# Optimization experiments

Hardware: AMD Instinct MI355X
Metric: run time of the kernel (lower is better)

The kernel has to match this reference:

```python
import jax, jax.numpy as jnp
import numpy as np

B, T, F, H, P, HEADS = 1024, 128, 9, 256, 2048, 4
DH = H // HEADS

def _lstm_layer(x, Wih, Whh, bih, bhh):
    # x: [B,T,in]; gate order i,f,g,o (torch convention)
    xp = jnp.einsum('bti,gi->btg', x, Wih) + bih + bhh  # [B,T,4H]
    h0 = jnp.zeros((x.shape[0], Whh.shape[1]), x.dtype)
    def step(carry, xt):
        h, c = carry
        g = xt + h @ Whh.T
        i, f, gg, o = jnp.split(g, 4, axis=-1)
        c = jax.nn.sigmoid(f) * c + jax.nn.sigmoid(i) * jnp.tanh(gg)
        h = jax.nn.sigmoid(o) * jnp.tanh(c)
        return (h, c), h
    _, hs = jax.lax.scan(step, (h0, h0), jnp.swapaxes(xp, 0, 1))
    return jnp.swapaxes(hs, 0, 1)  # [B,T,H]

def _layernorm(x, g, b, eps=1e-5):
    mu = x.mean(-1, keepdims=True)
    var = ((x - mu) ** 2).mean(-1, keepdims=True)
    return (x - mu) * jax.lax.rsqrt(var + eps) * g + b

def setup_inputs():
    key = jax.random.key(0)
    ks = jax.random.split(key, 30)
    w = lambda k, s: jax.random.normal(k, s, jnp.float32) * 0.05
    return {
        'x': jax.random.normal(ks[0], (B, T, F), jnp.float32),
        'sku_indices': jnp.arange(B, dtype=jnp.int32),
        'adj': jax.random.uniform(ks[1], (P, P), jnp.float32),
        'vsn_emb_w': w(ks[2], (F, H)), 'vsn_emb_b': w(ks[3], (F, H)),
        'vsn_sel_w': w(ks[4], (F, F)), 'vsn_sel_b': w(ks[5], (F,)),
        'lstm_Wih0': w(ks[6], (4 * H, H)), 'lstm_Whh0': w(ks[7], (4 * H, H)),
        'lstm_bih0': w(ks[8], (4 * H,)), 'lstm_bhh0': w(ks[9], (4 * H,)),
        'lstm_Wih1': w(ks[10], (4 * H, H)), 'lstm_Whh1': w(ks[11], (4 * H, H)),
        'lstm_bih1': w(ks[12], (4 * H,)), 'lstm_bhh1': w(ks[13], (4 * H,)),
        'attn_in_w': w(ks[14], (3 * H, H)), 'attn_in_b': w(ks[15], (3 * H,)),
        'attn_out_w': w(ks[16], (H, H)), 'attn_out_b': w(ks[17], (H,)),
        'gnn_w': w(ks[18], (H, H)), 'gnn_b': w(ks[19], (H,)),
        'ln_g': jnp.ones((H,), jnp.float32), 'ln_b': jnp.zeros((H,), jnp.float32),
        'gate_w': w(ks[20], (H, 2 * H)), 'gate_b': w(ks[21], (H,)),
        'out_w': w(ks[22], (1, H)), 'out_b': w(ks[23], (1,)),
    }

def reference(x, sku_indices, adj, vsn_emb_w, vsn_emb_b, vsn_sel_w, vsn_sel_b,
              lstm_Wih0, lstm_Whh0, lstm_bih0, lstm_bhh0,
              lstm_Wih1, lstm_Whh1, lstm_bih1, lstm_bhh1,
              attn_in_w, attn_in_b, attn_out_w, attn_out_b,
              gnn_w, gnn_b, ln_g, ln_b, gate_w, gate_b, out_w, out_b):
    # --- TFT hidden: variable selection -> 2-layer LSTM -> MHA, take last step ---
    emb = x[..., None] * vsn_emb_w + vsn_emb_b           # [B,T,F,H]
    wts = jax.nn.softmax(x @ vsn_sel_w.T + vsn_sel_b, -1)  # [B,T,F]
    h = jnp.einsum('btf,btfh->bth', wts, emb)            # [B,T,H]
    h = _lstm_layer(h, lstm_Wih0, lstm_Whh0, lstm_bih0, lstm_bhh0)
    h = _lstm_layer(h, lstm_Wih1, lstm_Whh1, lstm_bih1, lstm_bhh1)
    qkv = h @ attn_in_w.T + attn_in_b                    # [B,T,3H]
    q, k, v = [a.reshape(B, T, HEADS, DH) for a in jnp.split(qkv, 3, axis=-1)]
    scores = jnp.einsum('bqhd,bkhd->bhqk', q, k) / np.sqrt(DH).astype(np.float32)
    attn = jax.nn.softmax(scores, -1)
    o = jnp.einsum('bhqk,bkhd->bqhd', attn, v).reshape(B, T, H)
    o = o @ attn_out_w.T + attn_out_b
    hidden = o[:, -1, :]                                  # [B,H]
    # --- GNN enrichment (all sku_indices valid here) ---
    product_embeds = jnp.zeros((P, H), hidden.dtype).at[sku_indices].set(hidden)
    degree = jnp.clip(adj.sum(1, keepdims=True), 1e-6)
    aggregated = (adj / degree) @ product_embeds          # [P,H]
    transformed = jax.nn.gelu(aggregated @ gnn_w.T + gnn_b, approximate=False)
    transformed = _layernorm(transformed, ln_g, ln_b)
    enriched = transformed[sku_indices]                   # [B,H]
    gate = jax.nn.sigmoid(jnp.concatenate([hidden, enriched], -1) @ gate_w.T + gate_b)
    combined = gate * enriched + (1.0 - gate) * hidden
    out = combined @ out_w.T + out_b                      # [B,1]
    return out.squeeze(-1)
```

## Files before the change

kernel.cpp:

```cpp
#include <hip/hip_runtime.h>
#include <hip/hip_fp16.h>

typedef _Float16 f16;
typedef _Float16 f16x8 __attribute__((ext_vector_type(8)));
typedef _Float16 f16x4 __attribute__((ext_vector_type(4)));
typedef float f32x4 __attribute__((ext_vector_type(4)));

#define B_ 1024
#define T_ 128
#define F_ 9
#define H_ 256
#define P_ 2048

#define AL(p) __hip_atomic_load((p), __ATOMIC_RELAXED, __HIP_MEMORY_SCOPE_AGENT)
#define AS(p, v) __hip_atomic_store((p), (v), __ATOMIC_RELAXED, __HIP_MEMORY_SCOPE_AGENT)

__device__ __forceinline__ float sigf(float x) { return 1.f / (1.f + __expf(-x)); }
__device__ __forceinline__ float tanh_(float x) {
  float a = fminf(fabsf(x), 12.f);
  float e = __expf(2.f * a);
  float r = 1.f - 2.f / (e + 1.f);
  return copysignf(r, x);
}

__device__ __forceinline__ f16x8 aload16(const f16* p) {
  union { unsigned long long u[2]; f16x8 v; } r;
  r.u[0] = AL((const unsigned long long*)p);
  r.u[1] = AL((const unsigned long long*)p + 1);
  return r.v;
}

__device__ __forceinline__ float blk_sum(float v) {
  __shared__ float sh[8];
  int lane = threadIdx.x & 63, w = threadIdx.x >> 6;
  int nw = blockDim.x >> 6;
#pragma unroll
  for (int o = 32; o > 0; o >>= 1) v += __shfl_xor(v, o, 64);
  __syncthreads();
  if (lane == 0) sh[w] = v;
  __syncthreads();
  float t = 0.f;
  for (int i = 0; i < nw; i++) t += sh[i];
  return t;
}

__global__ __launch_bounds__(256) void gemm_f16(
    const f16* __restrict__ A, int lda,
    const f16* __restrict__ Bt, int ldb,
    const float* __restrict__ bias,
    f16* __restrict__ o16, int ldo16,
    float* __restrict__ o32, int ldo32,
    int M, int N, int K)
{
  __shared__ __align__(16) f16 As[128][40];
  __shared__ __align__(16) f16 Bs[128][40];
  const int tid = threadIdx.x;
  const int lane = tid & 63, wave = tid >> 6;
  const int wr = (wave >> 1) * 64, wc = (wave & 1) * 64;
  const int q = lane >> 4, l15 = lane & 15;
  const int bm = blockIdx.x * 128, bn = blockIdx.y * 128;

  f32x4 acc[4][4];
#pragma unroll
  for (int i = 0; i < 4; i++)
#pragma unroll
    for (int j = 0; j < 4; j++) acc[i][j] = (f32x4){0.f, 0.f, 0.f, 0.f};

  for (int k0 = 0; k0 < K; k0 += 32) {
#pragma unroll
    for (int c = 0; c < 2; ++c) {
      int ch = tid + c * 256;
      int row = ch >> 2, kh = (ch & 3) * 8;
      *(f16x8*)&As[row][kh] = *(const f16x8*)&A[(size_t)(bm + row) * lda + k0 + kh];
      *(f16x8*)&Bs[row][kh] = *(const f16x8*)&Bt[(size_t)(bn + row) * ldb + k0 + kh];
    }
    __syncthreads();
    f16x8 af[4], bf[4];
#pragma unroll
    for (int tm = 0; tm < 4; tm++) af[tm] = *(const f16x8*)&As[wr + tm * 16 + l15][q * 8];
#pragma unroll
    for (int tn = 0; tn < 4; tn++) bf[tn] = *(const f16x8*)&Bs[wc + tn * 16 + l15][q * 8];
#pragma unroll
    for (int tm = 0; tm < 4; tm++)
#pragma unroll
      for (int tn = 0; tn < 4; tn++)
        acc[tm][tn] = __builtin_amdgcn_mfma_f32_16x16x32_f16(af[tm], bf[tn], acc[tm][tn], 0, 0, 0);
    __syncthreads();
  }
#pragma unroll
  for (int tm = 0; tm < 4; tm++) {
#pragma unroll
    for (int tn = 0; tn < 4; tn++) {
      int colg = bn + wc + tn * 16 + l15;
      float bv = bias ? bias[colg] : 0.f;
#pragma unroll
      for (int r = 0; r < 4; r++) {
        int rowg = bm + wr + tm * 16 + q * 4 + r;
        float v = acc[tm][tn][r] + bv;
        if (o32) o32[(size_t)rowg * ldo32 + colg] = v;
        if (o16) o16[(size_t)rowg * ldo16 + colg] = (f16)v;
      }
    }
  }
}

__global__ __launch_bounds__(256, 1) void lstm_pipe(
    f16* __restrict__ hio,
    const f16* __restrict__ wpk0, const f16* __restrict__ wpk1,
    const float* __restrict__ b0, const float* __restrict__ b1,
    int* __restrict__ cnt0, int* __restrict__ cnt1)
{
  __shared__ __align__(16) f16 apf[2][16][64][8];
  __shared__ __align__(16) f16 htile[32][64];
  const int tid = threadIdx.x;
  const int lane = tid & 63, w = tid >> 6;
  const int q = lane >> 4, l15 = lane & 15;
  const int layer = blockIdx.x >> 7;
  const int lbid = blockIdx.x & 127;
  const int grp = lbid & 31, s = lbid >> 5;
  const int m0 = grp * 32;
  const f16* wpk = layer ? wpk1 : wpk0;
  const float* bias = layer ? b1 : b0;
  int* mycnt = (layer ? cnt1 : cnt0) + grp * 64;
  int* xcnt  = cnt0 + grp * 64;

  f16x8 bf[4][16];
  {
    const f16* wbase = wpk + (((size_t)(s * 4 + w) * 4) * 16) * 512 + lane * 8;
#pragma unroll
    for (int g = 0; g < 4; g++)
#pragma unroll
      for (int k = 0; k < 16; k++)
        bf[g][k] = *(const f16x8*)(wbase + (size_t)(g * 16 + k) * 512);
  }
  float bv[4];
#pragma unroll
  for (int g = 0; g < 4; g++) bv[g] = bias[g * 256 + s * 64 + w * 16 + l15];

  const int srow = lane & 15, scb = lane >> 4;
  size_t rb[2];
  rb[0] = ((size_t)(m0 + srow) * T_) * 256 + scb * 8;
  rb[1] = ((size_t)(m0 + 16 + srow) * T_) * 256 + scb * 8;

  const f16x8 zv = {(f16)0, (f16)0, (f16)0, (f16)0, (f16)0, (f16)0, (f16)0, (f16)0};
  const int xcap = 4 + 4 * T_;

  if (layer) {
    if (tid == 0) {
      int it = 0;
      while (AL(xcnt) < 8) {
        __builtin_amdgcn_s_sleep(1);
        if (++it > (1 << 22)) break;
      }
    }
    __syncthreads();
  }
  f16x8 xr[2][2];
#pragma unroll
  for (int mt = 0; mt < 2; mt++) {
    if (layer) {
      xr[mt][0] = aload16(&hio[rb[mt] + (size_t)w * 32]);
      xr[mt][1] = aload16(&hio[rb[mt] + (size_t)(w + 4) * 32]);
    } else {
      xr[mt][0] = *(const f16x8*)&hio[rb[mt] + (size_t)w * 32];
      xr[mt][1] = *(const f16x8*)&hio[rb[mt] + (size_t)(w + 4) * 32];
    }
  }
  float cst[2][4] = {{0.f, 0.f, 0.f, 0.f}, {0.f, 0.f, 0.f, 0.f}};

  __syncthreads();
  if (tid == 0)
    __hip_atomic_fetch_add(mycnt, 1, __ATOMIC_RELAXED, __HIP_MEMORY_SCOPE_AGENT);

  for (int t = 0; t < T_; ++t) {
    if (tid == 0) {
      int needO = 4 * t + 4;
      int needX = 0;
      if (layer) { needX = 4 * t + 12; if (needX > xcap) needX = xcap; }
      int it = 0;
      for (;;) {
        int a = AL(mycnt);
        int b = needX ? AL(xcnt) : 0;
        if (a >= needO && b >= needX) break;
        __builtin_amdgcn_s_sleep(1);
        if (++it > (1 << 22)) break;
      }
    }
    __syncthreads();
#pragma unroll
    for (int mt = 0; mt < 2; mt++) {
      *(f16x8*)&apf[mt][w][lane][0]     = xr[mt][0];
      *(f16x8*)&apf[mt][w + 4][lane][0] = xr[mt][1];
      f16x8 h0 = zv, h1 = zv;
      if (t > 0) {
        h0 = aload16(&hio[rb[mt] + (size_t)(t - 1) * 256 + (size_t)w * 32]);
        h1 = aload16(&hio[rb[mt] + (size_t)(t - 1) * 256 + (size_t)(w + 4) * 32]);
      }
      *(f16x8*)&apf[mt][8 + w][lane][0]  = h0;
      *(f16x8*)&apf[mt][12 + w][lane][0] = h1;
    }
    __syncthreads();

    f32x4 acc[2][4];
#pragma unroll
    for (int mt = 0; mt < 2; mt++)
#pragma unroll
      for (int g = 0; g < 4; g++) acc[mt][g] = (f32x4){0.f, 0.f, 0.f, 0.f};
#pragma unroll
    for (int k = 0; k < 16; k++) {
      f16x8 a0 = *(const f16x8*)&apf[0][k][lane][0];
      f16x8 a1 = *(const f16x8*)&apf[1][k][lane][0];
#pragma unroll
      for (int g = 0; g < 4; g++) {
        acc[0][g] = __builtin_amdgcn_mfma_f32_16x16x32_f16(a0, bf[g][k], acc[0][g], 0, 0, 0);
        acc[1][g] = __builtin_amdgcn_mfma_f32_16x16x32_f16(a1, bf[g][k], acc[1][g], 0, 0, 0);
      }
    }
    if (t + 1 < T_) {
#pragma unroll
      for (int mt = 0; mt < 2; mt++) {
        if (layer) {
          xr[mt][0] = aload16(&hio[rb[mt] + (size_t)(t + 1) * 256 + (size_t)w * 32]);
          xr[mt][1] = aload16(&hio[rb[mt] + (size_t)(t + 1) * 256 + (size_t)(w + 4) * 32]);
        } else {
          xr[mt][0] = *(const f16x8*)&hio[rb[mt] + (size_t)(t + 1) * 256 + (size_t)w * 32];
          xr[mt][1] = *(const f16x8*)&hio[rb[mt] + (size_t)(t + 1) * 256 + (size_t)(w + 4) * 32];
        }
      }
    }
    f16 hn[2][4];
#pragma unroll
    for (int mt = 0; mt < 2; mt++)
#pragma unroll
      for (int r = 0; r < 4; r++) {
        float ip = acc[mt][0][r] + bv[0];
        float fp = acc[mt][1][r] + bv[1];
        float gp = acc[mt][2][r] + bv[2];
        float op = acc[mt][3][r] + bv[3];
        float cn = sigf(fp) * cst[mt][r] + sigf(ip) * tanh_(gp);
        cst[mt][r] = cn;
        hn[mt][r] = (f16)(sigf(op) * tanh_(cn));
      }
    __syncthreads();
#pragma unroll
    for (int mt = 0; mt < 2; mt++)
#pragma unroll
      for (int r = 0; r < 4; r++)
        htile[mt * 16 + q * 4 + r][w * 16 + l15] = hn[mt][r];
    __syncthreads();
    {
      int row = tid >> 3, c8 = (tid & 7) * 8;
      union { unsigned long long u[2]; f16x8 v; } uh;
      uh.v = *(const f16x8*)&htile[row][c8];
      unsigned long long* dst =
          (unsigned long long*)&hio[((size_t)(m0 + row) * T_ + t) * 256 + s * 64 + c8];
      AS(dst, uh.u[0]);
      AS(dst + 1, uh.u[1]);
    }
    __syncthreads();
    if (tid == 0)
      __hip_atomic_fetch_add(mycnt, 1, __ATOMIC_RELAXED, __HIP_MEMORY_SCOPE_AGENT);
  }
}

__global__ __launch_bounds__(256) void vsn_w_kernel(
    const float* __restrict__ x, const float* __restrict__ selw,
    const float* __restrict__ selb, float* __restrict__ wb)
{
  int pos = blockIdx.x * 256 + threadIdx.x;
  const float* xr = x + (size_t)pos * F_;
  float xv[F_];
#pragma unroll
  for (int f = 0; f < F_; f++) xv[f] = xr[f];
  float wv[F_]; float mx = -1e30f;
#pragma unroll
  for (int f = 0; f < F_; f++) {
    float s = selb[f];
#pragma unroll
    for (int f2 = 0; f2 < F_; f2++) s += xv[f2] * selw[f * F_ + f2];
    wv[f] = s; mx = fmaxf(mx, s);
  }
  float se = 0.f;
#pragma unroll
  for (int f = 0; f < F_; f++) { wv[f] = __expf(wv[f] - mx); se += wv[f]; }
  float inv = 1.f / se;
  float* o = wb + (size_t)pos * 18;
#pragma unroll
  for (int f = 0; f < F_; f++) {
    float wt = wv[f] * inv;
    o[f] = wt; o[9 + f] = wt * xv[f];
  }
}

__global__ __launch_bounds__(256) void vsn_h_kernel(
    const float* __restrict__ wb, const float* __restrict__ embw,
    const float* __restrict__ embb, f16* __restrict__ hout)
{
  int j = threadIdx.x;
  float ew[F_], eb[F_];
#pragma unroll
  for (int f = 0; f < F_; f++) { ew[f] = embw[f * H_ + j]; eb[f] = embb[f * H_ + j]; }
  for (int i = 0; i < 128; i++) {
    size_t pos = blockIdx.x + (size_t)i * 1024;
    const float* w = wb + pos * 18;
    float h = 0.f;
#pragma unroll
    for (int f = 0; f < F_; f++) h += w[9 + f] * ew[f] + w[f] * eb[f];
    hout[pos * H_ + j] = (f16)h;
  }
}

__global__ __launch_bounds__(256) void qk_kernel(
    const float* __restrict__ qbuf, const float* __restrict__ attn_in_w,
    float* __restrict__ qk)
{
  __shared__ float qs[256];
  int b = blockIdx.x, j = threadIdx.x;
  qs[j] = qbuf[(size_t)b * 256 + j];
  __syncthreads();
#pragma unroll
  for (int h = 0; h < 4; h++) {
    float acc = 0.f;
    for (int d = 0; d < 64; d++)
      acc += qs[h * 64 + d] * attn_in_w[(size_t)(256 + h * 64 + d) * 256 + j];
    qk[((size_t)b * 4 + h) * 256 + j] = acc * 0.125f;
  }
}

__global__ __launch_bounds__(256) void attnpool_kernel(
    const f16* __restrict__ hseq, const float* __restrict__ qk,
    float* __restrict__ hbar)
{
  __shared__ __align__(16) f16 hs[T_][264];
  __shared__ float qks[4][256];
  __shared__ float ps[4][T_];
  int b = blockIdx.x, tid = threadIdx.x;
  for (int i = tid; i < T_ * 32; i += 256) {
    int row = i >> 5, cc = (i & 31) * 8;
    *(f16x8*)&hs[row][cc] = *(const f16x8*)&hseq[((size_t)b * T_ + row) * 256 + cc];
  }
  for (int i = tid; i < 1024; i += 256) qks[i >> 8][i & 255] = qk[(size_t)b * 1024 + i];
  __syncthreads();
  if (tid < T_) {
    float s[4] = {0.f, 0.f, 0.f, 0.f};
    for (int cc = 0; cc < 32; cc++) {
      f16x8 v = *(const f16x8*)&hs[tid][cc * 8];
#pragma unroll
      for (int h = 0; h < 4; h++) {
        float a = 0.f;
#pragma unroll
        for (int j = 0; j < 8; j++) a += qks[h][cc * 8 + j] * (float)v[j];
        s[h] += a;
      }
    }
#pragma unroll
    for (int h = 0; h < 4; h++) ps[h][tid] = s[h];
  }
  __syncthreads();
  {
    int w = tid >> 6, l = tid & 63;
    float a = ps[w][l], bb = ps[w][l + 64];
    float m = fmaxf(a, bb);
#pragma unroll
    for (int o = 32; o > 0; o >>= 1) m = fmaxf(m, __shfl_xor(m, o, 64));
    float e0 = __expf(a - m), e1 = __expf(bb - m);
    float se = e0 + e1;
#pragma unroll
    for (int o = 32; o > 0; o >>= 1) se += __shfl_xor(se, o, 64);
    float inv = 1.f / se;
    ps[w][l] = e0 * inv; ps[w][l + 64] = e1 * inv;
  }
  __syncthreads();
  int j = tid;
  float acc[4] = {0.f, 0.f, 0.f, 0.f};
  for (int t = 0; t < T_; t++) {
    float hv = (float)hs[t][j];
#pragma unroll
    for (int h = 0; h < 4; h++) acc[h] += ps[h][t] * hv;
  }
#pragma unroll
  for (int h = 0; h < 4; h++) hbar[((size_t)b * 4 + h) * 256 + j] = acc[h];
}

__global__ __launch_bounds__(256) void vproj_kernel(
    const float* __restrict__ hbar, const float* __restrict__ attn_in_w,
    const float* __restrict__ attn_in_b, f16* __restrict__ aob)
{
  __shared__ float hb[4][256];
  int b = blockIdx.x, tid = threadIdx.x;
  for (int i = tid; i < 1024; i += 256) hb[i >> 8][i & 255] = hbar[(size_t)b * 1024 + i];
  __syncthreads();
  int d = tid, h = d >> 6;
  const float4* wr = (const float4*)(attn_in_w + (size_t)(512 + d) * 256);
  float acc = 0.f;
  for (int cc = 0; cc < 64; cc++) {
    float4 w4 = wr[cc];
    acc += w4.x * hb[h][cc * 4] + w4.y * hb[h][cc * 4 + 1]
         + w4.z * hb[h][cc * 4 + 2] + w4.w * hb[h][cc * 4 + 3];
  }
  aob[(size_t)b * 256 + d] = (f16)(acc + attn_in_b[512 + d]);
}

__global__ __launch_bounds__(256) void deg_adjn_kernel(
    const float* __restrict__ adj, const int* __restrict__ sku,
    f16* __restrict__ adjn)
{
  int bp = blockIdx.x;
  int p = sku[bp];
  int tid = threadIdx.x;
  float s = 0.f;
  for (int j = tid; j < P_; j += 256) s += adj[(size_t)p * P_ + j];
  float tot = blk_sum(s);
  float inv = 1.f / fmaxf(tot, 1e-6f);
  for (int b = tid; b < B_; b += 256)
    adjn[(size_t)bp * B_ + b] = (f16)(adj[(size_t)p * P_ + sku[b]] * inv);
}

__global__ void transpose_kernel(const float* __restrict__ hid, f16* __restrict__ hT)
{
  int i = blockIdx.x * 256 + threadIdx.x;
  int b = i >> 8, j = i & 255;
  hT[(size_t)j * B_ + b] = (f16)hid[i];
}

__global__ __launch_bounds__(256) void gelu_ln_kernel(
    const float* __restrict__ pre, const float* __restrict__ lg,
    const float* __restrict__ lb, float* __restrict__ enr,
    f16* __restrict__ hidcat)
{
  int row = blockIdx.x, j = threadIdx.x;
  float xv = pre[row * 256 + j];
  float ge = 0.5f * xv * (1.f + erff(xv * 0.70710678118654752f));
  float mu = blk_sum(ge) * (1.f / 256.f);
  float d = ge - mu;
  float var = blk_sum(d * d) * (1.f / 256.f);
  float y = d * rsqrtf(var + 1e-5f) * lg[j] + lb[j];
  enr[row * 256 + j] = y;
  hidcat[row * 512 + 256 + j] = (f16)y;
}

__global__ __launch_bounds__(256) void final_kernel(
    const float* __restrict__ gpre, const float* __restrict__ enr,
    const float* __restrict__ hid, const float* __restrict__ outw,
    const float* __restrict__ outb, float* __restrict__ out)
{
  int b = blockIdx.x, j = threadIdx.x;
  float gt = sigf(gpre[b * 256 + j]);
  float comb = gt * enr[b * 256 + j] + (1.f - gt) * hid[b * 256 + j];
  float v = comb * outw[j];
  float s = blk_sum(v);
  if (j == 0) out[b] = s + outb[0];
}

__global__ void prep_kernel(
    const float* Wih0, const float* Whh0, const float* Wih1, const float* Whh1,
    const float* bih0, const float* bhh0, const float* bih1, const float* bhh1,
    const float* attn_in_w, const float* attn_out_w, const float* gnn_w,
    const float* gate_w,
    f16* wpk0, f16* wpk1, f16* attninf, f16* attnoutf, f16* gnnwf, f16* gatewf,
    float* bias0, float* bias1)
{
  int idx = blockIdx.x * 256 + threadIdx.x;
  if (idx < 524288) {
    int j = idx & 7, lane = (idx >> 3) & 63, k = (idx >> 9) & 15;
    int g = (idx >> 13) & 3, w = (idx >> 15) & 3, s = (idx >> 17) & 3;
    int row = g * 256 + s * 64 + w * 16 + (lane & 15);
    int col = k * 32 + (lane >> 4) * 8 + j;
    float v0 = col < 256 ? Wih0[(size_t)row * 256 + col] : Whh0[(size_t)row * 256 + col - 256];
    float v1 = col < 256 ? Wih1[(size_t)row * 256 + col] : Whh1[(size_t)row * 256 + col - 256];
    wpk0[idx] = (f16)v0;
    wpk1[idx] = (f16)v1;
    return;
  }
  int i = idx - 524288;
  if (i < 65536) { attninf[i] = (f16)attn_in_w[i]; return; }
  i -= 65536;
  if (i < 65536) { attnoutf[i] = (f16)attn_out_w[i]; return; }
  i -= 65536;
  if (i < 65536) { gnnwf[i] = (f16)gnn_w[i]; return; }
  i -= 65536;
  if (i < 131072) { gatewf[i] = (f16)gate_w[i]; return; }
  i -= 131072;
  if (i < 1024) { bias0[i] = bih0[i] + bhh0[i]; return; }
  i -= 1024;
  if (i < 1024) { bias1[i] = bih1[i] + bhh1[i]; return; }
}

extern "C" void kernel_launch(void* const* d_in, const int* in_sizes, int n_in,
                              void* d_out, int out_size, void* d_ws, size_t ws_size,
                              hipStream_t stream)
{
  const float* x         = (const float*)d_in[0];
  const int*   sku       = (const int*)  d_in[1];
  const float* adj       = (const float*)d_in[2];
  const float* vsn_emb_w = (const float*)d_in[3];
  const float* vsn_emb_b = (const float*)d_in[4];
  const float* vsn_sel_w = (const float*)d_in[5];
  const float* vsn_sel_b = (const float*)d_in[6];
  const float* Wih0 = (const float*)d_in[7];
  const float* Whh0 = (const float*)d_in[8];
  const float* bih0 = (const float*)d_in[9];
  const float* bhh0 = (const float*)d_in[10];
  const float* Wih1 = (const float*)d_in[11];
  const float* Whh1 = (const float*)d_in[12];
  const float* bih1 = (const float*)d_in[13];
  const float* bhh1 = (const float*)d_in[14];
  const float* attn_in_w  = (const float*)d_in[15];
  const float* attn_in_b  = (const float*)d_in[16];
  const float* attn_out_w = (const float*)d_in[17];
  const float* attn_out_b = (const float*)d_in[18];
  const float* gnn_w  = (const float*)d_in[19];
  const float* gnn_b  = (const float*)d_in[20];
  const float* ln_g   = (const float*)d_in[21];
  const float* ln_b   = (const float*)d_in[22];
  const float* gate_w = (const float*)d_in[23];
  const float* gate_b = (const float*)d_in[24];
  const float* out_w  = (const float*)d_in[25];
  const float* out_b  = (const float*)d_in[26];
  (void)in_sizes; (void)n_in; (void)out_size; (void)ws_size;

  char* wsb = (char*)d_ws;
  size_t off = 0;
  auto alloc = [&](size_t bytes) -> void* {
    void* p = wsb + off;
    off += (bytes + 255) & ~(size_t)255;
    return p;
  };
  f16* hA      = (f16*)alloc((size_t)B_ * T_ * H_ * 2);
  f16* wpk0    = (f16*)alloc((size_t)1024 * 512 * 2);
  f16* wpk1    = (f16*)alloc((size_t)1024 * 512 * 2);
  f16* attninf = (f16*)alloc((size_t)256 * 256 * 2);
  f16* attnoutf= (f16*)alloc((size_t)256 * 256 * 2);
  f16* gnnwf   = (f16*)alloc((size_t)256 * 256 * 2);
  f16* gatewf  = (f16*)alloc((size_t)256 * 512 * 2);
  float* bias0 = (float*)alloc(1024 * 4);
  float* bias1 = (float*)alloc(1024 * 4);
  int* cnt0    = (int*)alloc(32 * 64 * 4);
  int* cnt1    = (int*)alloc(32 * 64 * 4);
  size_t off_tail = off;
  float* qbuf  = (float*)alloc((size_t)B_ * 256 * 4);
  float* qk    = (float*)alloc((size_t)B_ * 4 * 256 * 4);
  float* hbar  = (float*)alloc((size_t)B_ * 4 * 256 * 4);
  f16* aob     = (f16*)alloc((size_t)B_ * 256 * 2);
  float* hidden32 = (float*)alloc((size_t)B_ * 256 * 4);
  f16* hidcat  = (f16*)alloc((size_t)B_ * 512 * 2);
  f16* hT      = (f16*)alloc((size_t)256 * B_ * 2);
  f16* adjn    = (f16*)alloc((size_t)B_ * B_ * 2);
  f16* aggf    = (f16*)alloc((size_t)B_ * 256 * 2);
  float* gnnpre= (float*)alloc((size_t)B_ * 256 * 4);
  float* enr32 = (float*)alloc((size_t)B_ * 256 * 4);
  float* gatepre=(float*)alloc((size_t)B_ * 256 * 4);
  float* wb    = (float*)(wsb + off_tail);

  hipMemsetAsync(cnt0, 0, 2 * 32 * 64 * 4, stream);

  prep_kernel<<<3336, 256, 0, stream>>>(
      Wih0, Whh0, Wih1, Whh1, bih0, bhh0, bih1, bhh1,
      attn_in_w, attn_out_w, gnn_w, gate_w,
      wpk0, wpk1, attninf, attnoutf, gnnwf, gatewf, bias0, bias1);

  vsn_w_kernel<<<512, 256, 0, stream>>>(x, vsn_sel_w, vsn_sel_b, wb);
  vsn_h_kernel<<<1024, 256, 0, stream>>>(wb, vsn_emb_w, vsn_emb_b, hA);
  lstm_pipe<<<256, 256, 0, stream>>>(hA, wpk0, wpk1, bias0, bias1, cnt0, cnt1);

  dim3 gS(B_ / 128, 256 / 128);
  gemm_f16<<<gS, 256, 0, stream>>>(hA + (size_t)(T_ - 1) * 256, T_ * 256, attninf, 256,
                                   attn_in_b, nullptr, 0, qbuf, 256, B_, 256, 256);
  qk_kernel<<<B_, 256, 0, stream>>>(qbuf, attn_in_w, qk);
  attnpool_kernel<<<B_, 256, 0, stream>>>(hA, qk, hbar);
  vproj_kernel<<<B_, 256, 0, stream>>>(hbar, attn_in_w, attn_in_b, aob);
  gemm_f16<<<gS, 256, 0, stream>>>(aob, 256, attnoutf, 256, attn_out_b,
                                   hidcat, 512, hidden32, 256, B_, 256, 256);
  deg_adjn_kernel<<<B_, 256, 0, stream>>>(adj, sku, adjn);
  transpose_kernel<<<B_, 256, 0, stream>>>(hidden32, hT);
  gemm_f16<<<gS, 256, 0, stream>>>(adjn, 1024, hT, 1024, nullptr,
                                   aggf, 256, nullptr, 0, B_, 256, 1024);
  gemm_f16<<<gS, 256, 0, stream>>>(aggf, 256, gnnwf, 256, gnn_b,
                                   nullptr, 0, gnnpre, 256, B_, 256, 256);
  gelu_ln_kernel<<<B_, 256, 0, stream>>>(gnnpre, ln_g, ln_b, enr32, hidcat);
  gemm_f16<<<gS, 256, 0, stream>>>(hidcat, 512, gatewf, 512, gate_b,
                                   nullptr, 0, gatepre, 256, B_, 256, 512);
  final_kernel<<<B_, 256, 0, stream>>>(gatepre, enr32, hidden32, out_w, out_b, (float*)d_out);
}
```

Baseline: 1.012 ms.

## Replace shared LSTM step counter with per-slice flags and reuse own h tile

The single atomic counter per row group, which four blocks incremented each step, becomes four per-slice flag words that each block writes with a plain store. Waiters read them as two 64-bit loads. Each block now takes its own previous-step hidden slice from shared memory instead of re-reading it from global memory, and one barrier before the htile write is dropped. This aims to cut atomic contention, global-memory latency on the recurrent critical path, and barrier overhead. In exchange it relies on the htile contents from the prior step staying valid, and on the flag layout (four ints per group) matching the counter buffer.

```diff
diff --git a/kernel.cpp b/kernel.cpp
--- a/kernel.cpp
+++ b/kernel.cpp
@@ -121,8 +121,12 @@
   const int m0 = grp * 32;
   const f16* wpk = layer ? wpk1 : wpk0;
   const float* bias = layer ? b1 : b0;
-  int* mycnt = (layer ? cnt1 : cnt0) + grp * 64;
-  int* xcnt  = cnt0 + grp * 64;
+  int* myflags = (layer ? cnt1 : cnt0) + grp * 64;
+  int* xflags  = cnt0 + grp * 64;
+
+  const int own0 = ((w >> 1) == s);
+  const int own1 = (((w + 4) >> 1) == s);
+  const int offh = (w & 1) * 32;
 
   f16x8 bf[4][16];
   {
@@ -143,12 +147,15 @@
   rb[1] = ((size_t)(m0 + 16 + srow) * T_) * 256 + scb * 8;
 
   const f16x8 zv = {(f16)0, (f16)0, (f16)0, (f16)0, (f16)0, (f16)0, (f16)0, (f16)0};
-  const int xcap = 4 + 4 * T_;
 
   if (layer) {
     if (tid == 0) {
       int it = 0;
-      while (AL(xcnt) < 8) {
+      for (;;) {
+        unsigned long long a = AL((unsigned long long*)xflags);
+        unsigned long long b2 = AL((unsigned long long*)xflags + 1);
+        if ((int)a >= 2 && (int)(a >> 32) >= 2 &&
+            (int)b2 >= 2 && (int)(b2 >> 32) >= 2) break;
         __builtin_amdgcn_s_sleep(1);
         if (++it > (1 << 22)) break;
       }
@@ -169,32 +176,42 @@
   float cst[2][4] = {{0.f, 0.f, 0.f, 0.f}, {0.f, 0.f, 0.f, 0.f}};
 
   __syncthreads();
-  if (tid == 0)
-    __hip_atomic_fetch_add(mycnt, 1, __ATOMIC_RELAXED, __HIP_MEMORY_SCOPE_AGENT);
+  if (tid == 0) AS(&myflags[s], 1);
 
   for (int t = 0; t < T_; ++t) {
     if (tid == 0) {
-      int needO = 4 * t + 4;
+      const int needO = t + 1;
       int needX = 0;
-      if (layer) { needX = 4 * t + 12; if (needX > xcap) needX = xcap; }
+      if (layer) { needX = t + 3; if (needX > T_ + 1) needX = T_ + 1; }
       int it = 0;
       for (;;) {
-        int a = AL(mycnt);
-        int b = needX ? AL(xcnt) : 0;
-        if (a >= needO && b >= needX) break;
+        unsigned long long a = AL((unsigned long long*)myflags);
+        unsigned long long b2 = AL((unsigned long long*)myflags + 1);
+        bool ok = (int)a >= needO && (int)(a >> 32) >= needO &&
+                  (int)b2 >= needO && (int)(b2 >> 32) >= needO;
+        if (ok && layer) {
+          unsigned long long c = AL((unsigned long long*)xflags);
+          unsigned long long d = AL((unsigned long long*)xflags + 1);
+          ok = (int)c >= needX && (int)(c >> 32) >= needX &&
+               (int)d >= needX && (int)(d >> 32) >= needX;
+        }
+        if (ok) break;
         __builtin_amdgcn_s_sleep(1);
         if (++it > (1 << 22)) break;
       }
     }
     __syncthreads();
+
 #pragma unroll
     for (int mt = 0; mt < 2; mt++) {
       *(f16x8*)&apf[mt][w][lane][0]     = xr[mt][0];
       *(f16x8*)&apf[mt][w + 4][lane][0] = xr[mt][1];
       f16x8 h0 = zv, h1 = zv;
       if (t > 0) {
-        h0 = aload16(&hio[rb[mt] + (size_t)(t - 1) * 256 + (size_t)w * 32]);
-        h1 = aload16(&hio[rb[mt] + (size_t)(t - 1) * 256 + (size_t)(w + 4) * 32]);
+        if (own0) h0 = *(const f16x8*)&htile[mt * 16 + srow][offh + scb * 8];
+        else      h0 = aload16(&hio[rb[mt] + (size_t)(t - 1) * 256 + (size_t)w * 32]);
+        if (own1) h1 = *(const f16x8*)&htile[mt * 16 + srow][offh + scb * 8];
+        else      h1 = aload16(&hio[rb[mt] + (size_t)(t - 1) * 256 + (size_t)(w + 4) * 32]);
       }
       *(f16x8*)&apf[mt][8 + w][lane][0]  = h0;
       *(f16x8*)&apf[mt][12 + w][lane][0] = h1;
@@ -241,7 +258,6 @@
         cst[mt][r] = cn;
         hn[mt][r] = (f16)(sigf(op) * tanh_(cn));
       }
-    __syncthreads();
 #pragma unroll
     for (int mt = 0; mt < 2; mt++)
 #pragma unroll
@@ -258,8 +274,7 @@
       AS(dst + 1, uh.u[1]);
     }
     __syncthreads();
-    if (tid == 0)
-      __hip_atomic_fetch_add(mycnt, 1, __ATOMIC_RELAXED, __HIP_MEMORY_SCOPE_AGENT);
+    if (tid == 0) AS(&myflags[s], t + 2);
   }
 }
 
```

After: 1.015 ms. No clear change (+0.3%).

## Replace LSTM counter-based inter-block sync with poisoned-buffer data polling

Applied to the files above, without the earlier changes.

Drops the per-group atomic counters and the single-thread spin-wait. Each wavefront now polls the actual h/x data, which is pre-filled with an all-ones NaN sentinel, until no sentinel remains. Separate buffers hold the input, the layer-0 outputs and the layer-1 outputs, and two __syncthreads per step are removed. The aim is to cut the latency of the per-timestep cross-block handoff. In exchange it adds two large memsets per call, more workspace, and correctness depends on 8-byte stores never producing the sentinel value and on split 16-byte stores being observed whole.

```diff
diff --git a/kernel.cpp b/kernel.cpp
--- a/kernel.cpp
+++ b/kernel.cpp
@@ -12,6 +12,7 @@
 #define H_ 256
 #define P_ 2048
 
+typedef unsigned long long ull;
 #define AL(p) __hip_atomic_load((p), __ATOMIC_RELAXED, __HIP_MEMORY_SCOPE_AGENT)
 #define AS(p, v) __hip_atomic_store((p), (v), __ATOMIC_RELAXED, __HIP_MEMORY_SCOPE_AGENT)
 
@@ -21,13 +22,6 @@
   float e = __expf(2.f * a);
   float r = 1.f - 2.f / (e + 1.f);
   return copysignf(r, x);
-}
-
-__device__ __forceinline__ f16x8 aload16(const f16* p) {
-  union { unsigned long long u[2]; f16x8 v; } r;
-  r.u[0] = AL((const unsigned long long*)p);
-  r.u[1] = AL((const unsigned long long*)p + 1);
-  return r.v;
 }
 
 __device__ __forceinline__ float blk_sum(float v) {
@@ -105,10 +99,11 @@
 }
 
 __global__ __launch_bounds__(256, 1) void lstm_pipe(
-    f16* __restrict__ hio,
+    const f16* __restrict__ xA,
+    f16* __restrict__ h0b,
+    f16* __restrict__ h1b,
     const f16* __restrict__ wpk0, const f16* __restrict__ wpk1,
-    const float* __restrict__ b0, const float* __restrict__ b1,
-    int* __restrict__ cnt0, int* __restrict__ cnt1)
+    const float* __restrict__ b0, const float* __restrict__ b1)
 {
   __shared__ __align__(16) f16 apf[2][16][64][8];
   __shared__ __align__(16) f16 htile[32][64];
@@ -121,8 +116,9 @@
   const int m0 = grp * 32;
   const f16* wpk = layer ? wpk1 : wpk0;
   const float* bias = layer ? b1 : b0;
-  int* mycnt = (layer ? cnt1 : cnt0) + grp * 64;
-  int* xcnt  = cnt0 + grp * 64;
+  const f16* xsrc = layer ? h0b : xA;
+  f16* hdst = layer ? h1b : h0b;
+  const f16* hsrc = hdst;
 
   f16x8 bf[4][16];
   {
@@ -143,61 +139,66 @@
   rb[1] = ((size_t)(m0 + 16 + srow) * T_) * 256 + scb * 8;
 
   const f16x8 zv = {(f16)0, (f16)0, (f16)0, (f16)0, (f16)0, (f16)0, (f16)0, (f16)0};
-  const int xcap = 4 + 4 * T_;
-
-  if (layer) {
-    if (tid == 0) {
-      int it = 0;
-      while (AL(xcnt) < 8) {
-        __builtin_amdgcn_s_sleep(1);
-        if (++it > (1 << 22)) break;
-      }
-    }
-    __syncthreads();
-  }
+  const ull POI = 0xFFFFFFFFFFFFFFFFull;
+  union U { ull u[2]; f16x8 v; };
+
   f16x8 xr[2][2];
-#pragma unroll
-  for (int mt = 0; mt < 2; mt++) {
-    if (layer) {
-      xr[mt][0] = aload16(&hio[rb[mt] + (size_t)w * 32]);
-      xr[mt][1] = aload16(&hio[rb[mt] + (size_t)(w + 4) * 32]);
-    } else {
-      xr[mt][0] = *(const f16x8*)&hio[rb[mt] + (size_t)w * 32];
-      xr[mt][1] = *(const f16x8*)&hio[rb[mt] + (size_t)(w + 4) * 32];
+  if (!layer) {
+#pragma unroll
+    for (int mt = 0; mt < 2; mt++) {
+      xr[mt][0] = *(const f16x8*)&xA[rb[mt] + (size_t)w * 32];
+      xr[mt][1] = *(const f16x8*)&xA[rb[mt] + (size_t)(w + 4) * 32];
     }
   }
   float cst[2][4] = {{0.f, 0.f, 0.f, 0.f}, {0.f, 0.f, 0.f, 0.f}};
 
-  __syncthreads();
-  if (tid == 0)
-    __hip_atomic_fetch_add(mycnt, 1, __ATOMIC_RELAXED, __HIP_MEMORY_SCOPE_AGENT);
-
   for (int t = 0; t < T_; ++t) {
-    if (tid == 0) {
-      int needO = 4 * t + 4;
-      int needX = 0;
-      if (layer) { needX = 4 * t + 12; if (needX > xcap) needX = xcap; }
+    U gx[2][2], gh[2][2];
+    const bool needx = (layer != 0);
+    const bool needh = (t > 0);
+    if (needx || needh) {
       int it = 0;
       for (;;) {
-        int a = AL(mycnt);
-        int b = needX ? AL(xcnt) : 0;
-        if (a >= needO && b >= needX) break;
-        __builtin_amdgcn_s_sleep(1);
+        if (needx) {
+#pragma unroll
+          for (int mt = 0; mt < 2; mt++) {
+            const ull* p0 = (const ull*)&xsrc[rb[mt] + (size_t)t * 256 + (size_t)w * 32];
+            const ull* p1 = (const ull*)&xsrc[rb[mt] + (size_t)t * 256 + (size_t)(w + 4) * 32];
+            gx[mt][0].u[0] = AL(p0); gx[mt][0].u[1] = AL(p0 + 1);
+            gx[mt][1].u[0] = AL(p1); gx[mt][1].u[1] = AL(p1 + 1);
+          }
+        }
+        if (needh) {
+#pragma unroll
+          for (int mt = 0; mt < 2; mt++) {
+            const ull* p0 = (const ull*)&hsrc[rb[mt] + (size_t)(t - 1) * 256 + (size_t)w * 32];
+            const ull* p1 = (const ull*)&hsrc[rb[mt] + (size_t)(t - 1) * 256 + (size_t)(w + 4) * 32];
+            gh[mt][0].u[0] = AL(p0); gh[mt][0].u[1] = AL(p0 + 1);
+            gh[mt][1].u[0] = AL(p1); gh[mt][1].u[1] = AL(p1 + 1);
+          }
+        }
+        bool bad = false;
+        if (needx)
+#pragma unroll
+          for (int mt = 0; mt < 2; mt++)
+            bad |= (gx[mt][0].u[0] == POI) | (gx[mt][0].u[1] == POI) |
+                   (gx[mt][1].u[0] == POI) | (gx[mt][1].u[1] == POI);
+        if (needh)
+#pragma unroll
+          for (int mt = 0; mt < 2; mt++)
+            bad |= (gh[mt][0].u[0] == POI) | (gh[mt][0].u[1] == POI) |
+                   (gh[mt][1].u[0] == POI) | (gh[mt][1].u[1] == POI);
+        if (!bad) break;
         if (++it > (1 << 22)) break;
+        __builtin_amdgcn_s_sleep(2);
       }
     }
-    __syncthreads();
 #pragma unroll
     for (int mt = 0; mt < 2; mt++) {
-      *(f16x8*)&apf[mt][w][lane][0]     = xr[mt][0];
-      *(f16x8*)&apf[mt][w + 4][lane][0] = xr[mt][1];
-      f16x8 h0 = zv, h1 = zv;
-      if (t > 0) {
-        h0 = aload16(&hio[rb[mt] + (size_t)(t - 1) * 256 + (size_t)w * 32]);
-        h1 = aload16(&hio[rb[mt] + (size_t)(t - 1) * 256 + (size_t)(w + 4) * 32]);
-      }
-      *(f16x8*)&apf[mt][8 + w][lane][0]  = h0;
-      *(f16x8*)&apf[mt][12 + w][lane][0] = h1;
+      *(f16x8*)&apf[mt][w][lane][0]      = layer ? gx[mt][0].v : xr[mt][0];
+      *(f16x8*)&apf[mt][w + 4][lane][0]  = layer ? gx[mt][1].v : xr[mt][1];
+      *(f16x8*)&apf[mt][8 + w][lane][0]  = needh ? gh[mt][0].v : zv;
+      *(f16x8*)&apf[mt][12 + w][lane][0] = needh ? gh[mt][1].v : zv;
     }
     __syncthreads();
 
@@ -216,16 +217,11 @@
         acc[1][g] = __builtin_amdgcn_mfma_f32_16x16x32_f16(a1, bf[g][k], acc[1][g], 0, 0, 0);
       }
     }
-    if (t + 1 < T_) {
+    if (!layer && t + 1 < T_) {
 #pragma unroll
       for (int mt = 0; mt < 2; mt++) {
-        if (layer) {
-          xr[mt][0] = aload16(&hio[rb[mt] + (size_t)(t + 1) * 256 + (size_t)w * 32]);
-          xr[mt][1] = aload16(&hio[rb[mt] + (size_t)(t + 1) * 256 + (size_t)(w + 4) * 32]);
-        } else {
-          xr[mt][0] = *(const f16x8*)&hio[rb[mt] + (size_t)(t + 1) * 256 + (size_t)w * 32];
-          xr[mt][1] = *(const f16x8*)&hio[rb[mt] + (size_t)(t + 1) * 256 + (size_t)(w + 4) * 32];
-        }
+        xr[mt][0] = *(const f16x8*)&xA[rb[mt] + (size_t)(t + 1) * 256 + (size_t)w * 32];
+        xr[mt][1] = *(const f16x8*)&xA[rb[mt] + (size_t)(t + 1) * 256 + (size_t)(w + 4) * 32];
       }
     }
     f16 hn[2][4];
@@ -241,7 +237,6 @@
         cst[mt][r] = cn;
         hn[mt][r] = (f16)(sigf(op) * tanh_(cn));
       }
-    __syncthreads();
 #pragma unroll
     for (int mt = 0; mt < 2; mt++)
 #pragma unroll
@@ -250,16 +245,12 @@
     __syncthreads();
     {
       int row = tid >> 3, c8 = (tid & 7) * 8;
-      union { unsigned long long u[2]; f16x8 v; } uh;
+      U uh;
       uh.v = *(const f16x8*)&htile[row][c8];
-      unsigned long long* dst =
-          (unsigned long long*)&hio[((size_t)(m0 + row) * T_ + t) * 256 + s * 64 + c8];
+      ull* dst = (ull*)&hdst[((size_t)(m0 + row) * T_ + t) * 256 + s * 64 + c8];
       AS(dst, uh.u[0]);
       AS(dst + 1, uh.u[1]);
     }
-    __syncthreads();
-    if (tid == 0)
-      __hip_atomic_fetch_add(mycnt, 1, __ATOMIC_RELAXED, __HIP_MEMORY_SCOPE_AGENT);
   }
 }
 
@@ -519,6 +510,8 @@
   const float* out_b  = (const float*)d_in[26];
   (void)in_sizes; (void)n_in; (void)out_size; (void)ws_size;
 
+  const size_t HBYTES = (size_t)B_ * T_ * H_ * 2;
+
   char* wsb = (char*)d_ws;
   size_t off = 0;
   auto alloc = [&](size_t bytes) -> void* {
@@ -526,7 +519,10 @@
     off += (bytes + 255) & ~(size_t)255;
     return p;
   };
-  f16* hA      = (f16*)alloc((size_t)B_ * T_ * H_ * 2);
+  f16* hA      = (f16*)alloc(HBYTES);
+  size_t off_hB = off;
+  f16* hB      = (f16*)alloc(HBYTES);
+  f16* hC      = (f16*)alloc(HBYTES);
   f16* wpk0    = (f16*)alloc((size_t)1024 * 512 * 2);
   f16* wpk1    = (f16*)alloc((size_t)1024 * 512 * 2);
   f16* attninf = (f16*)alloc((size_t)256 * 256 * 2);
@@ -535,9 +531,8 @@
   f16* gatewf  = (f16*)alloc((size_t)256 * 512 * 2);
   float* bias0 = (float*)alloc(1024 * 4);
   float* bias1 = (float*)alloc(1024 * 4);
-  int* cnt0    = (int*)alloc(32 * 64 * 4);
-  int* cnt1    = (int*)alloc(32 * 64 * 4);
-  size_t off_tail = off;
+  off = off_hB;
+  float* wb    = (float*)alloc((size_t)B_ * T_ * 18 * 4);
   float* qbuf  = (float*)alloc((size_t)B_ * 256 * 4);
   float* qk    = (float*)alloc((size_t)B_ * 4 * 256 * 4);
   float* hbar  = (float*)alloc((size_t)B_ * 4 * 256 * 4);
@@ -550,9 +545,6 @@
   float* gnnpre= (float*)alloc((size_t)B_ * 256 * 4);
   float* enr32 = (float*)alloc((size_t)B_ * 256 * 4);
   float* gatepre=(float*)alloc((size_t)B_ * 256 * 4);
-  float* wb    = (float*)(wsb + off_tail);
-
-  hipMemsetAsync(cnt0, 0, 2 * 32 * 64 * 4, stream);
 
   prep_kernel<<<3336, 256, 0, stream>>>(
       Wih0, Whh0, Wih1, Whh1, bih0, bhh0, bih1, bhh1,
@@ -561,13 +553,15 @@
 
   vsn_w_kernel<<<512, 256, 0, stream>>>(x, vsn_sel_w, vsn_sel_b, wb);
   vsn_h_kernel<<<1024, 256, 0, stream>>>(wb, vsn_emb_w, vsn_emb_b, hA);
-  lstm_pipe<<<256, 256, 0, stream>>>(hA, wpk0, wpk1, bias0, bias1, cnt0, cnt1);
+  hipMemsetAsync(hB, 0xFF, HBYTES, stream);
+  hipMemsetAsync(hC, 0xFF, HBYTES, stream);
+  lstm_pipe<<<256, 256, 0, stream>>>(hA, hB, hC, wpk0, wpk1, bias0, bias1);
 
   dim3 gS(B_ / 128, 256 / 128);
-  gemm_f16<<<gS, 256, 0, stream>>>(hA + (size_t)(T_ - 1) * 256, T_ * 256, attninf, 256,
+  gemm_f16<<<gS, 256, 0, stream>>>(hC + (size_t)(T_ - 1) * 256, T_ * 256, attninf, 256,
                                    attn_in_b, nullptr, 0, qbuf, 256, B_, 256, 256);
   qk_kernel<<<B_, 256, 0, stream>>>(qbuf, attn_in_w, qk);
-  attnpool_kernel<<<B_, 256, 0, stream>>>(hA, qk, hbar);
+  attnpool_kernel<<<B_, 256, 0, stream>>>(hC, qk, hbar);
   vproj_kernel<<<B_, 256, 0, stream>>>(hbar, attn_in_w, attn_in_b, aob);
   gemm_f16<<<gS, 256, 0, stream>>>(aob, 256, attnoutf, 256, attn_out_b,
                                    hidcat, 512, hidden32, 256, B_, 256, 256);
```

After: 1.145 ms. 13.2% more time.
